# Performance work log

Measured on AMD Instinct MI355X. Metric: run time of the kernel, lower is better.

The kernel has to match this reference:

```python
import jax, jax.numpy as jnp
import numpy as np

COMMITMENT_COST = 0.25


def setup_inputs() -> dict:
    key = jax.random.key(0)
    k1, k2 = jax.random.split(key)
    B, H, W, D, K = 64, 32, 32, 64, 512
    inputs = jax.random.normal(k1, (B, H, W, D), dtype=jnp.float32)
    # VarianceScaling(): truncated normal with stddev ~ sqrt(1/fan_in); plain normal scaled is fine as init
    embeddings = jax.random.normal(k2, (D, K), dtype=jnp.float32) * np.float32(1.0 / np.sqrt(D))
    return {"inputs": inputs, "embeddings": embeddings}


def reference(inputs, embeddings):
    D = embeddings.shape[0]
    flat = inputs.reshape(-1, D)  # [N, D]
    distances = (
        jnp.sum(flat * flat, axis=1, keepdims=True)
        - 2.0 * (flat @ embeddings)
        + jnp.sum(embeddings * embeddings, axis=0, keepdims=True)
    )
    encoding_indices = jnp.argmin(distances, axis=1)  # [N]
    # one-hot @ embeddings.T is just a gather of rows of embeddings.T
    quantized = jnp.take(embeddings.T, encoding_indices, axis=0).reshape(inputs.shape)
    loss = (
        jnp.mean(jnp.square(jax.lax.stop_gradient(quantized) - inputs))
        + COMMITMENT_COST * jnp.mean(jnp.square(quantized - jax.lax.stop_gradient(inputs)))
    )
    # straight-through estimator
    quantized_st = inputs + jax.lax.stop_gradient(quantized - inputs)
    indices = encoding_indices.reshape(inputs.shape[:-1])
    return quantized_st, indices, loss
```

## Files before the change

### kernel.cpp

```cpp
#include <hip/hip_runtime.h>
#include <stdint.h>


#define DDIM 64
#define KCODES 512

typedef __bf16 bf16x8 __attribute__((ext_vector_type(8)));
typedef float f32x4 __attribute__((ext_vector_type(4)));


__device__ __forceinline__ void split3(float f, __bf16& h1, __bf16& h2,
                                       __bf16& h3) {
  h1 = (__bf16)f;
  float r1 = f - (float)h1;
  h2 = (__bf16)r1;
  float r2 = r1 - (float)h2;
  h3 = (__bf16)r2;
}

__global__ void vq_prep_m(const float* __restrict__ w,
                          bf16x8* __restrict__ wb,
                          float* __restrict__ wT, float* __restrict__ wsq,
                          float* __restrict__ loss_out) {
  const int b = blockIdx.x, t = threadIdx.x;
  if (b < 16) {
    const int c = b * 256 + t;
    const int ctg = c >> 7;
    const int h = (c >> 6) & 1;
    const int L = c & 63, quad = L >> 4, col = L & 15;
    bf16x8 v1, v2, v3;
#pragma unroll
    for (int j = 0; j < 8; ++j) {
      float f = w[(quad * 8 + 32 * h + j) * KCODES + ctg * 16 + col];
      __bf16 h1, h2, h3; split3(f, h1, h2, h3);
      v1[j] = h1; v2[j] = h2; v3[j] = h3;
    }
    wb[c] = v1; wb[4096 + c] = v2; wb[8192 + c] = v3;
  } else {
    int g = (b - 16) * 256 + t;
    int d = g >> 9, k = g & 511;
    wT[k * DDIM + d] = w[g];
    if (g < KCODES) {
      float s = 0.f;
      for (int dd = 0; dd < DDIM; ++dd) {
        float tv = w[dd * KCODES + g];
        s = fmaf(tv, tv, s);
      }
      wsq[g] = s;
    }
    if (g == 0) *loss_out = 0.f;
  }
}

__global__ __launch_bounds__(256, 2)
void vq_mfma(const float* __restrict__ x_in, const bf16x8* __restrict__ wb,
             const float* __restrict__ wsq, const float* __restrict__ wT,
             float* __restrict__ out_q, float* __restrict__ out_idx,
             float* __restrict__ loss_out) {
  __shared__ bf16x8 ldsb[3072];
  __shared__ unsigned long long sm_key[128];
  __shared__ float sm_xsq[128];
  __shared__ unsigned int sm_idx[128];
  __shared__ float sm_loss[128];

  const int t = threadIdx.x, b = blockIdx.x;
  const int wv = t >> 6, L = t & 63, quad = L >> 4, col = L & 15;

  bf16x8 a[2][3][2];
#pragma unroll
  for (int as = 0; as < 2; ++as) {
    const float* xr =
        x_in + ((size_t)b * 128 + (wv * 2 + as) * 16 + col) * DDIM + quad * 8;
    float ssq = 0.f;
#pragma unroll
    for (int h = 0; h < 2; ++h) {
      float4 p0 = *(const float4*)(xr + 32 * h);
      float4 p1 = *(const float4*)(xr + 32 * h + 4);
      float f[8] = {p0.x, p0.y, p0.z, p0.w, p1.x, p1.y, p1.z, p1.w};
      bf16x8 v1, v2, v3;
#pragma unroll
      for (int j = 0; j < 8; ++j) {
        ssq = fmaf(f[j], f[j], ssq);
        __bf16 h1, h2, h3; split3(f[j], h1, h2, h3);
        v1[j] = h1; v2[j] = h2; v3[j] = h3;
      }
      a[as][0][h] = v1; a[as][1][h] = v2; a[as][2][h] = v3;
    }
    ssq += __shfl_xor(ssq, 16, 64);
    ssq += __shfl_xor(ssq, 32, 64);
    if (quad == 0) sm_xsq[wv * 32 + as * 16 + col] = ssq;
  }

  float best[2][4];
  int bidx[2][4];
#pragma unroll
  for (int as = 0; as < 2; ++as)
#pragma unroll
    for (int r = 0; r < 4; ++r) { best[as][r] = 3.0e38f; bidx[as][r] = 0; }

#pragma unroll 1
  for (int ph = 0; ph < 4; ++ph) {
    __syncthreads();
#pragma unroll
    for (int i = 0; i < 12; ++i) {
      int idx = i * 256 + t;
      int chunk = idx >> 6, Ls = idx & 63;
      int ct = chunk / 6, r6 = chunk % 6;
      int h = r6 / 3, s = r6 % 3;
      ldsb[chunk * 64 + Ls] = wb[s * 4096 + ((ph * 8 + ct) * 2 + h) * 64 + Ls];
    }
    __syncthreads();
#pragma unroll 1
    for (int ct = 0; ct < 8; ++ct) {
      f32x4 acc0 = {0.f, 0.f, 0.f, 0.f};
      f32x4 acc1 = {0.f, 0.f, 0.f, 0.f};
#pragma unroll
      for (int h = 0; h < 2; ++h) {
        bf16x8 b0 = ldsb[(ct * 6 + h * 3 + 0) * 64 + L];
        bf16x8 b1 = ldsb[(ct * 6 + h * 3 + 1) * 64 + L];
        bf16x8 b2 = ldsb[(ct * 6 + h * 3 + 2) * 64 + L];
        acc0 = __builtin_amdgcn_mfma_f32_16x16x32_bf16(a[0][0][h], b0, acc0, 0, 0, 0);
        acc1 = __builtin_amdgcn_mfma_f32_16x16x32_bf16(a[1][0][h], b0, acc1, 0, 0, 0);
        acc0 = __builtin_amdgcn_mfma_f32_16x16x32_bf16(a[0][0][h], b1, acc0, 0, 0, 0);
        acc1 = __builtin_amdgcn_mfma_f32_16x16x32_bf16(a[1][0][h], b1, acc1, 0, 0, 0);
        acc0 = __builtin_amdgcn_mfma_f32_16x16x32_bf16(a[0][1][h], b0, acc0, 0, 0, 0);
        acc1 = __builtin_amdgcn_mfma_f32_16x16x32_bf16(a[1][1][h], b0, acc1, 0, 0, 0);
        acc0 = __builtin_amdgcn_mfma_f32_16x16x32_bf16(a[0][1][h], b1, acc0, 0, 0, 0);
        acc1 = __builtin_amdgcn_mfma_f32_16x16x32_bf16(a[1][1][h], b1, acc1, 0, 0, 0);
        acc0 = __builtin_amdgcn_mfma_f32_16x16x32_bf16(a[0][0][h], b2, acc0, 0, 0, 0);
        acc1 = __builtin_amdgcn_mfma_f32_16x16x32_bf16(a[1][0][h], b2, acc1, 0, 0, 0);
        acc0 = __builtin_amdgcn_mfma_f32_16x16x32_bf16(a[0][2][h], b0, acc0, 0, 0, 0);
        acc1 = __builtin_amdgcn_mfma_f32_16x16x32_bf16(a[1][2][h], b0, acc1, 0, 0, 0);
      }
      int code = ph * 128 + ct * 16 + col;
      float wq = wsq[code];
#pragma unroll
      for (int r = 0; r < 4; ++r) {
        float d0 = fmaf(acc0[r], -2.0f, wq);
        if (d0 < best[0][r]) { best[0][r] = d0; bidx[0][r] = code; }
        float d1 = fmaf(acc1[r], -2.0f, wq);
        if (d1 < best[1][r]) { best[1][r] = d1; bidx[1][r] = code; }
      }
    }
  }

#pragma unroll
  for (int as = 0; as < 2; ++as) {
#pragma unroll
    for (int r = 0; r < 4; ++r) {
      unsigned int ub = __float_as_uint(best[as][r]);
      ub = (ub & 0x80000000u) ? ~ub : (ub | 0x80000000u);
      unsigned long long key = ((unsigned long long)ub << 32) |
                               (unsigned long long)(unsigned int)bidx[as][r];
#pragma unroll
      for (int off = 1; off < 16; off <<= 1) {
        unsigned long long o = __shfl_xor(key, off, 64);
        key = o < key ? o : key;
      }
      if (col == 0)
        sm_key[wv * 32 + as * 16 + quad * 4 + r] = key;
    }
  }
  __syncthreads();

  if (t < 128) {
    unsigned long long k = sm_key[t];
    unsigned int idx = (unsigned int)k;
    sm_idx[t] = idx;
    out_idx[(size_t)b * 128 + t] = (float)idx;
    unsigned int u = (unsigned int)(k >> 32);
    u = (u & 0x80000000u) ? (u & 0x7FFFFFFFu) : ~u;
    sm_loss[t] = (__uint_as_float(u) + sm_xsq[t]) * (1.25f / 4194304.0f);
  }
  __syncthreads();

  float4* dst = (float4*)(out_q + (size_t)b * 8192);
#pragma unroll
  for (int i = 0; i < 8; ++i) {
    int e4 = i * 256 + t;
    int p2 = e4 >> 4, d4 = e4 & 15;
    unsigned int idx = sm_idx[p2];
    dst[e4] = ((const float4*)(wT + (size_t)idx * DDIM))[d4];
  }

  if (t < 64) {
    float s = sm_loss[t] + sm_loss[t + 64];
#pragma unroll
    for (int off = 32; off > 0; off >>= 1) s += __shfl_down(s, off);
    if (t == 0) atomicAdd(loss_out, s);
  }
}


__global__ void vq_prep(const float* __restrict__ w, float* __restrict__ wT,
                        float* __restrict__ wsq, float* __restrict__ loss_out) {
  int g = blockIdx.x * 256 + threadIdx.x;
  int d = g >> 9, k = g & 511;
  wT[k * DDIM + d] = w[g];
  if (g < KCODES) {
    float s = 0.f;
    for (int dd = 0; dd < DDIM; ++dd) {
      float t = w[dd * KCODES + g];
      s = fmaf(t, t, s);
    }
    wsq[g] = s;
  }
  if (g == 0) *loss_out = 0.f;
}

__global__ __launch_bounds__(512, 8)
void vq_main(const float* __restrict__ x_in, const float* __restrict__ w,
             const float* __restrict__ wT, const float* __restrict__ wsq,
             float* __restrict__ out_q, float* __restrict__ out_idx,
             float* __restrict__ loss_out) {
  __shared__ float xs[DDIM][65];
  __shared__ unsigned long long sm_key[8][64];
  __shared__ unsigned int sm_idx[64];
  __shared__ float sm_sx[64];
  __shared__ float sm_loss[64];

  const int t = threadIdx.x;
  const int pb = blockIdx.x;
  const int wv = __builtin_amdgcn_readfirstlane(t >> 6);
  const int lane = t & 63;

  {
    const float4* src = (const float4*)(x_in + (size_t)pb * 4096);
#pragma unroll
    for (int i = 0; i < 2; ++i) {
      int e4 = i * 512 + t;
      float4 v = src[e4];
      int e = e4 << 2;
      int pt = e >> 6, d = e & 63;
      xs[d][pt] = v.x; xs[d + 1][pt] = v.y;
      xs[d + 2][pt] = v.z; xs[d + 3][pt] = v.w;
    }
  }
  __syncthreads();

  const int kbase = wv << 6;
  float best = 3.0e38f;
  int bidx = 0;
  float sx = 0.f;

#pragma unroll 1
  for (int kb = 0; kb < 2; ++kb) {
    const int k0 = kbase + (kb << 5);
    const float* wp = w + k0;
    float acc[32];
#pragma unroll
    for (int c = 0; c < 32; ++c) acc[c] = 0.f;
#pragma unroll 1
    for (int d8 = 0; d8 < 8; ++d8) {
      float xv[8];
#pragma unroll
      for (int dd = 0; dd < 8; ++dd) xv[dd] = xs[(d8 << 3) + dd][lane];
      if (wv == 0 && kb == 0) {
#pragma unroll
        for (int dd = 0; dd < 8; ++dd) sx = fmaf(xv[dd], xv[dd], sx);
      }
#pragma unroll
      for (int dd = 0; dd < 8; ++dd) {
        const float* wd = wp + (((d8 << 3) + dd) << 9);
#pragma unroll
        for (int c = 0; c < 32; ++c) acc[c] = fmaf(wd[c], xv[dd], acc[c]);
      }
    }
#pragma unroll
    for (int c = 0; c < 32; ++c) {
      float dist = fmaf(acc[c], -2.0f, wsq[k0 + c]);
      if (dist < best) { best = dist; bidx = k0 + c; }
    }
  }

  unsigned int ub = __float_as_uint(best);
  ub = (ub & 0x80000000u) ? ~ub : (ub | 0x80000000u);
  sm_key[wv][lane] =
      ((unsigned long long)ub << 32) | (unsigned long long)(unsigned int)bidx;
  if (wv == 0) sm_sx[lane] = sx;
  __syncthreads();

  if (t < 64) {
    unsigned long long k = sm_key[0][t];
#pragma unroll
    for (int wi = 1; wi < 8; ++wi) {
      unsigned long long k2 = sm_key[wi][t];
      k = k2 < k ? k2 : k;
    }
    unsigned int idx = (unsigned int)k;
    sm_idx[t] = idx;
    out_idx[((size_t)pb << 6) + t] = (float)idx;
    unsigned int u = (unsigned int)(k >> 32);
    u = (u & 0x80000000u) ? (u & 0x7FFFFFFFu) : ~u;
    sm_loss[t] = (__uint_as_float(u) + sm_sx[t]) * (1.25f / 4194304.0f);
  }
  __syncthreads();

  float4* dst = (float4*)(out_q + (size_t)pb * 4096);
#pragma unroll
  for (int i = 0; i < 2; ++i) {
    int e4 = i * 512 + t;
    int p2 = e4 >> 4, d4 = e4 & 15;
    unsigned int idx = sm_idx[p2];
    dst[e4] = ((const float4*)(wT + (size_t)idx * DDIM))[d4];
  }

  if (t < 64) {
    float s = sm_loss[t];
#pragma unroll
    for (int off = 32; off > 0; off >>= 1) s += __shfl_down(s, off);
    if (t == 0) atomicAdd(loss_out, s);
  }
}

extern "C" void kernel_launch(void* const* d_in, const int* in_sizes, int n_in,
                              void* d_out, int out_size, void* d_ws, size_t ws_size,
                              hipStream_t stream) {
  const float* x = (const float*)d_in[0];
  const float* w = (const float*)d_in[1];

  float* out_q = (float*)d_out;
  float* out_idx = out_q + 4194304;
  float* loss_out = out_q + 4259840;

  char* ws = (char*)d_ws;
  if (ws_size >= 329728) {
    bf16x8* wbp = (bf16x8*)(ws);
    float* wT = (float*)(ws + 196608);
    float* wsq = (float*)(ws + 327680);
    vq_prep_m<<<144, 256, 0, stream>>>(w, wbp, wT, wsq, loss_out);
    vq_mfma<<<512, 256, 0, stream>>>(x, wbp, wsq, wT, out_q, out_idx,
                                     loss_out);
  } else {
    float* wT = (float*)(ws);
    float* wsq = (float*)(ws + 131072);
    vq_prep<<<128, 256, 0, stream>>>(w, wT, wsq, loss_out);
    vq_main<<<1024, 512, 0, stream>>>(x, w, wT, wsq, out_q, out_idx,
                                      loss_out);
  }
}
```

Baseline: 107.6 us.

## Double-buffer codebook tiles in LDS with register prefetch and phase-ordered layout

Reorders the prepared bf16 codebook so each 64-code phase sits in one contiguous block. The main kernel now double-buffers that block in LDS: the next phase is prefetched into registers while MFMAs run on the current buffer, then written to the other buffer. This removes one barrier per phase and hides the global-load latency. It also hoists the wsq loads and raises wave priority during the MFMA section. The cost is higher register use for the prefetch (6 float4 per thread) and twice as many phase iterations, each with a smaller tile.

Result: no change. 109.7 us (+2.0%).

```diff
diff --git a/kernel.cpp b/kernel.cpp
--- a/kernel.cpp
+++ b/kernel.cpp
@@ -35,7 +35,10 @@
       __bf16 h1, h2, h3; split3(f, h1, h2, h3);
       v1[j] = h1; v2[j] = h2; v3[j] = h3;
     }
-    wb[c] = v1; wb[4096 + c] = v2; wb[8192 + c] = v3;
+    const int base = (ctg >> 2) * 24 + (ctg & 3) * 6 + h * 3;
+    wb[(base + 0) * 64 + L] = v1;
+    wb[(base + 1) * 64 + L] = v2;
+    wb[(base + 2) * 64 + L] = v3;
   } else {
     int g = (b - 16) * 256 + t;
     int d = g >> 9, k = g & 511;
@@ -66,6 +69,13 @@
   const int t = threadIdx.x, b = blockIdx.x;
   const int wv = t >> 6, L = t & 63, quad = L >> 4, col = L & 15;
 
+  const float4* wb4 = (const float4*)wb;
+  const int sgbase = wv * 64 + L;
+
+  float4 g[6];
+#pragma unroll
+  for (int i = 0; i < 6; ++i) g[i] = wb4[sgbase + i * 256];
+
   bf16x8 a[2][3][2];
 #pragma unroll
   for (int as = 0; as < 2; ++as) {
@@ -91,6 +101,10 @@
     if (quad == 0) sm_xsq[wv * 32 + as * 16 + col] = ssq;
   }
 
+#pragma unroll
+  for (int i = 0; i < 6; ++i)
+    *(float4*)&ldsb[sgbase + i * 256] = g[i];
+
   float best[2][4];
   int bidx[2][4];
 #pragma unroll
@@ -99,26 +113,28 @@
     for (int r = 0; r < 4; ++r) { best[as][r] = 3.0e38f; bidx[as][r] = 0; }
 
 #pragma unroll 1
-  for (int ph = 0; ph < 4; ++ph) {
+  for (int ph = 0; ph < 8; ++ph) {
     __syncthreads();
-#pragma unroll
-    for (int i = 0; i < 12; ++i) {
-      int idx = i * 256 + t;
-      int chunk = idx >> 6, Ls = idx & 63;
-      int ct = chunk / 6, r6 = chunk % 6;
-      int h = r6 / 3, s = r6 % 3;
-      ldsb[chunk * 64 + Ls] = wb[s * 4096 + ((ph * 8 + ct) * 2 + h) * 64 + Ls];
-    }
-    __syncthreads();
-#pragma unroll 1
-    for (int ct = 0; ct < 8; ++ct) {
+    float wq[4];
+#pragma unroll
+    for (int ct = 0; ct < 4; ++ct) wq[ct] = wsq[ph * 64 + ct * 16 + col];
+    if (ph < 7) {
+#pragma unroll
+      for (int i = 0; i < 6; ++i)
+        g[i] = wb4[(ph + 1) * 1536 + sgbase + i * 256];
+    }
+
+    const bf16x8* bufp = ldsb + (ph & 1) * 1536;
+    __builtin_amdgcn_s_setprio(1);
+#pragma unroll
+    for (int ct = 0; ct < 4; ++ct) {
       f32x4 acc0 = {0.f, 0.f, 0.f, 0.f};
       f32x4 acc1 = {0.f, 0.f, 0.f, 0.f};
 #pragma unroll
       for (int h = 0; h < 2; ++h) {
-        bf16x8 b0 = ldsb[(ct * 6 + h * 3 + 0) * 64 + L];
-        bf16x8 b1 = ldsb[(ct * 6 + h * 3 + 1) * 64 + L];
-        bf16x8 b2 = ldsb[(ct * 6 + h * 3 + 2) * 64 + L];
+        bf16x8 b0 = bufp[(ct * 6 + h * 3 + 0) * 64 + L];
+        bf16x8 b1 = bufp[(ct * 6 + h * 3 + 1) * 64 + L];
+        bf16x8 b2 = bufp[(ct * 6 + h * 3 + 2) * 64 + L];
         acc0 = __builtin_amdgcn_mfma_f32_16x16x32_bf16(a[0][0][h], b0, acc0, 0, 0, 0);
         acc1 = __builtin_amdgcn_mfma_f32_16x16x32_bf16(a[1][0][h], b0, acc1, 0, 0, 0);
         acc0 = __builtin_amdgcn_mfma_f32_16x16x32_bf16(a[0][0][h], b1, acc0, 0, 0, 0);
@@ -132,15 +148,20 @@
         acc0 = __builtin_amdgcn_mfma_f32_16x16x32_bf16(a[0][2][h], b0, acc0, 0, 0, 0);
         acc1 = __builtin_amdgcn_mfma_f32_16x16x32_bf16(a[1][2][h], b0, acc1, 0, 0, 0);
       }
-      int code = ph * 128 + ct * 16 + col;
-      float wq = wsq[code];
+      int code = ph * 64 + ct * 16 + col;
 #pragma unroll
       for (int r = 0; r < 4; ++r) {
-        float d0 = fmaf(acc0[r], -2.0f, wq);
+        float d0 = fmaf(acc0[r], -2.0f, wq[ct]);
         if (d0 < best[0][r]) { best[0][r] = d0; bidx[0][r] = code; }
-        float d1 = fmaf(acc1[r], -2.0f, wq);
+        float d1 = fmaf(acc1[r], -2.0f, wq[ct]);
         if (d1 < best[1][r]) { best[1][r] = d1; bidx[1][r] = code; }
       }
+    }
+    __builtin_amdgcn_s_setprio(0);
+    if (ph < 7) {
+#pragma unroll
+      for (int i = 0; i < 6; ++i)
+        *(float4*)&ldsb[((ph + 1) & 1) * 1536 + sgbase + i * 256] = g[i];
     }
   }
 
```

## Stream codebook fragments from global into registers with double buffering, drop LDS staging

Applied to the files above, without the earlier changes.

The prep kernel now stores the split-bf16 codebook fragments in per-code-tile contiguous order. This lets the main MFMA kernel load each tile's six fragments straight from global/L2 into a register double buffer, replacing the LDS staging and the syncthreads barriers. The MFMA chain is split into two independent accumulators per row set to shorten dependency chains, and the codebook squared-norm computation moves to extra parallel blocks using a shuffle reduction. Every wave now reads the codebook from cache instead of sharing it through LDS, which raises L2 traffic and register pressure.

New measurement: 96.36 us. -10.4%, faster.

```diff
diff --git a/kernel.cpp b/kernel.cpp
--- a/kernel.cpp
+++ b/kernel.cpp
@@ -35,20 +35,27 @@
       __bf16 h1, h2, h3; split3(f, h1, h2, h3);
       v1[j] = h1; v2[j] = h2; v3[j] = h3;
     }
-    wb[c] = v1; wb[4096 + c] = v2; wb[8192 + c] = v3;
-  } else {
+    const int base = (ctg >> 2) * 24 + (ctg & 3) * 6 + h * 3;
+    wb[(base + 0) * 64 + L] = v1;
+    wb[(base + 1) * 64 + L] = v2;
+    wb[(base + 2) * 64 + L] = v3;
+  } else if (b < 144) {
     int g = (b - 16) * 256 + t;
     int d = g >> 9, k = g & 511;
     wT[k * DDIM + d] = w[g];
-    if (g < KCODES) {
-      float s = 0.f;
-      for (int dd = 0; dd < DDIM; ++dd) {
-        float tv = w[dd * KCODES + g];
-        s = fmaf(tv, tv, s);
-      }
-      wsq[g] = s;
-    }
     if (g == 0) *loss_out = 0.f;
+  } else {
+    int i = (b - 144) * 256 + t;
+    int k = i >> 2, p = i & 3;
+    float s = 0.f;
+#pragma unroll
+    for (int dd = 0; dd < 16; ++dd) {
+      float tv = w[(p * 16 + dd) * KCODES + k];
+      s = fmaf(tv, tv, s);
+    }
+    s += __shfl_xor(s, 1, 64);
+    s += __shfl_xor(s, 2, 64);
+    if (p == 0) wsq[k] = s;
   }
 }
 
@@ -57,7 +64,6 @@
              const float* __restrict__ wsq, const float* __restrict__ wT,
              float* __restrict__ out_q, float* __restrict__ out_idx,
              float* __restrict__ loss_out) {
-  __shared__ bf16x8 ldsb[3072];
   __shared__ unsigned long long sm_key[128];
   __shared__ float sm_xsq[128];
   __shared__ unsigned int sm_idx[128];
@@ -65,6 +71,10 @@
 
   const int t = threadIdx.x, b = blockIdx.x;
   const int wv = t >> 6, L = t & 63, quad = L >> 4, col = L & 15;
+
+  bf16x8 bb[2][6];
+#pragma unroll
+  for (int j = 0; j < 6; ++j) bb[0][j] = wb[j * 64 + L];
 
   bf16x8 a[2][3][2];
 #pragma unroll
@@ -98,49 +108,57 @@
 #pragma unroll
     for (int r = 0; r < 4; ++r) { best[as][r] = 3.0e38f; bidx[as][r] = 0; }
 
-#pragma unroll 1
-  for (int ph = 0; ph < 4; ++ph) {
-    __syncthreads();
-#pragma unroll
-    for (int i = 0; i < 12; ++i) {
-      int idx = i * 256 + t;
-      int chunk = idx >> 6, Ls = idx & 63;
-      int ct = chunk / 6, r6 = chunk % 6;
-      int h = r6 / 3, s = r6 % 3;
-      ldsb[chunk * 64 + Ls] = wb[s * 4096 + ((ph * 8 + ct) * 2 + h) * 64 + Ls];
-    }
-    __syncthreads();
-#pragma unroll 1
-    for (int ct = 0; ct < 8; ++ct) {
-      f32x4 acc0 = {0.f, 0.f, 0.f, 0.f};
-      f32x4 acc1 = {0.f, 0.f, 0.f, 0.f};
-#pragma unroll
-      for (int h = 0; h < 2; ++h) {
-        bf16x8 b0 = ldsb[(ct * 6 + h * 3 + 0) * 64 + L];
-        bf16x8 b1 = ldsb[(ct * 6 + h * 3 + 1) * 64 + L];
-        bf16x8 b2 = ldsb[(ct * 6 + h * 3 + 2) * 64 + L];
-        acc0 = __builtin_amdgcn_mfma_f32_16x16x32_bf16(a[0][0][h], b0, acc0, 0, 0, 0);
-        acc1 = __builtin_amdgcn_mfma_f32_16x16x32_bf16(a[1][0][h], b0, acc1, 0, 0, 0);
-        acc0 = __builtin_amdgcn_mfma_f32_16x16x32_bf16(a[0][0][h], b1, acc0, 0, 0, 0);
-        acc1 = __builtin_amdgcn_mfma_f32_16x16x32_bf16(a[1][0][h], b1, acc1, 0, 0, 0);
-        acc0 = __builtin_amdgcn_mfma_f32_16x16x32_bf16(a[0][1][h], b0, acc0, 0, 0, 0);
-        acc1 = __builtin_amdgcn_mfma_f32_16x16x32_bf16(a[1][1][h], b0, acc1, 0, 0, 0);
-        acc0 = __builtin_amdgcn_mfma_f32_16x16x32_bf16(a[0][1][h], b1, acc0, 0, 0, 0);
-        acc1 = __builtin_amdgcn_mfma_f32_16x16x32_bf16(a[1][1][h], b1, acc1, 0, 0, 0);
-        acc0 = __builtin_amdgcn_mfma_f32_16x16x32_bf16(a[0][0][h], b2, acc0, 0, 0, 0);
-        acc1 = __builtin_amdgcn_mfma_f32_16x16x32_bf16(a[1][0][h], b2, acc1, 0, 0, 0);
-        acc0 = __builtin_amdgcn_mfma_f32_16x16x32_bf16(a[0][2][h], b0, acc0, 0, 0, 0);
-        acc1 = __builtin_amdgcn_mfma_f32_16x16x32_bf16(a[1][2][h], b0, acc1, 0, 0, 0);
-      }
-      int code = ph * 128 + ct * 16 + col;
-      float wq = wsq[code];
-#pragma unroll
-      for (int r = 0; r < 4; ++r) {
-        float d0 = fmaf(acc0[r], -2.0f, wq);
-        if (d0 < best[0][r]) { best[0][r] = d0; bidx[0][r] = code; }
-        float d1 = fmaf(acc1[r], -2.0f, wq);
-        if (d1 < best[1][r]) { best[1][r] = d1; bidx[1][r] = code; }
-      }
+#pragma unroll 2
+  for (int kk = 0; kk < 32; ++kk) {
+    const int cur = kk & 1, nxt = cur ^ 1;
+    if (kk < 31) {
+#pragma unroll
+      for (int j = 0; j < 6; ++j)
+        bb[nxt][j] = wb[(kk + 1) * 384 + j * 64 + L];
+    }
+    float wq = wsq[kk * 16 + col];
+
+    f32x4 aA0 = {0.f, 0.f, 0.f, 0.f}, aB0 = {0.f, 0.f, 0.f, 0.f};
+    f32x4 aA1 = {0.f, 0.f, 0.f, 0.f}, aB1 = {0.f, 0.f, 0.f, 0.f};
+    {
+      bf16x8 b0 = bb[cur][0], b1 = bb[cur][1], b2 = bb[cur][2];
+      aA0 = __builtin_amdgcn_mfma_f32_16x16x32_bf16(a[0][0][0], b0, aA0, 0, 0, 0);
+      aA1 = __builtin_amdgcn_mfma_f32_16x16x32_bf16(a[1][0][0], b0, aA1, 0, 0, 0);
+      aA0 = __builtin_amdgcn_mfma_f32_16x16x32_bf16(a[0][0][0], b1, aA0, 0, 0, 0);
+      aA1 = __builtin_amdgcn_mfma_f32_16x16x32_bf16(a[1][0][0], b1, aA1, 0, 0, 0);
+      aA0 = __builtin_amdgcn_mfma_f32_16x16x32_bf16(a[0][1][0], b0, aA0, 0, 0, 0);
+      aA1 = __builtin_amdgcn_mfma_f32_16x16x32_bf16(a[1][1][0], b0, aA1, 0, 0, 0);
+      aA0 = __builtin_amdgcn_mfma_f32_16x16x32_bf16(a[0][1][0], b1, aA0, 0, 0, 0);
+      aA1 = __builtin_amdgcn_mfma_f32_16x16x32_bf16(a[1][1][0], b1, aA1, 0, 0, 0);
+      aA0 = __builtin_amdgcn_mfma_f32_16x16x32_bf16(a[0][0][0], b2, aA0, 0, 0, 0);
+      aA1 = __builtin_amdgcn_mfma_f32_16x16x32_bf16(a[1][0][0], b2, aA1, 0, 0, 0);
+      aA0 = __builtin_amdgcn_mfma_f32_16x16x32_bf16(a[0][2][0], b0, aA0, 0, 0, 0);
+      aA1 = __builtin_amdgcn_mfma_f32_16x16x32_bf16(a[1][2][0], b0, aA1, 0, 0, 0);
+    }
+    {
+      bf16x8 b0 = bb[cur][3], b1 = bb[cur][4], b2 = bb[cur][5];
+      aB0 = __builtin_amdgcn_mfma_f32_16x16x32_bf16(a[0][0][1], b0, aB0, 0, 0, 0);
+      aB1 = __builtin_amdgcn_mfma_f32_16x16x32_bf16(a[1][0][1], b0, aB1, 0, 0, 0);
+      aB0 = __builtin_amdgcn_mfma_f32_16x16x32_bf16(a[0][0][1], b1, aB0, 0, 0, 0);
+      aB1 = __builtin_amdgcn_mfma_f32_16x16x32_bf16(a[1][0][1], b1, aB1, 0, 0, 0);
+      aB0 = __builtin_amdgcn_mfma_f32_16x16x32_bf16(a[0][1][1], b0, aB0, 0, 0, 0);
+      aB1 = __builtin_amdgcn_mfma_f32_16x16x32_bf16(a[1][1][1], b0, aB1, 0, 0, 0);
+      aB0 = __builtin_amdgcn_mfma_f32_16x16x32_bf16(a[0][1][1], b1, aB0, 0, 0, 0);
+      aB1 = __builtin_amdgcn_mfma_f32_16x16x32_bf16(a[1][1][1], b1, aB1, 0, 0, 0);
+      aB0 = __builtin_amdgcn_mfma_f32_16x16x32_bf16(a[0][0][1], b2, aB0, 0, 0, 0);
+      aB1 = __builtin_amdgcn_mfma_f32_16x16x32_bf16(a[1][0][1], b2, aB1, 0, 0, 0);
+      aB0 = __builtin_amdgcn_mfma_f32_16x16x32_bf16(a[0][2][1], b0, aB0, 0, 0, 0);
+      aB1 = __builtin_amdgcn_mfma_f32_16x16x32_bf16(a[1][2][1], b0, aB1, 0, 0, 0);
+    }
+    f32x4 acc0 = aA0 + aB0;
+    f32x4 acc1 = aA1 + aB1;
+    int code = kk * 16 + col;
+#pragma unroll
+    for (int r = 0; r < 4; ++r) {
+      float d0 = fmaf(acc0[r], -2.0f, wq);
+      if (d0 < best[0][r]) { best[0][r] = d0; bidx[0][r] = code; }
+      float d1 = fmaf(acc1[r], -2.0f, wq);
+      if (d1 < best[1][r]) { best[1][r] = d1; bidx[1][r] = code; }
     }
   }
 
@@ -328,7 +346,7 @@
     bf16x8* wbp = (bf16x8*)(ws);
     float* wT = (float*)(ws + 196608);
     float* wsq = (float*)(ws + 327680);
-    vq_prep_m<<<144, 256, 0, stream>>>(w, wbp, wT, wsq, loss_out);
+    vq_prep_m<<<152, 256, 0, stream>>>(w, wbp, wT, wsq, loss_out);
     vq_mfma<<<512, 256, 0, stream>>>(x, wbp, wsq, wT, out_q, out_idx,
                                      loss_out);
   } else {
```
